# Optimization experiments

Hardware: AMD Instinct MI355X
Metric: run time of the kernel (lower is better)

## Reference

```python
import jax, jax.numpy as jnp
import numpy as np

DIM, INNER, HEADS = 512, 64, 8

def setup_inputs() -> dict:
    key = jax.random.key(0)
    ks = jax.random.split(key, 9)
    s = lambda fan_in: 1.0 / np.sqrt(fan_in)
    x  = jax.random.normal(ks[0], (2, 4096, DIM), dtype=jnp.float32)
    # per-head Q/K/V projection weights (naive per-head linears in the source)
    Wq = jax.random.uniform(ks[1], (HEADS, DIM, INNER), minval=-s(DIM), maxval=s(DIM))
    Wk = jax.random.uniform(ks[2], (HEADS, DIM, INNER), minval=-s(DIM), maxval=s(DIM))
    Wv = jax.random.uniform(ks[3], (HEADS, DIM, INNER), minval=-s(DIM), maxval=s(DIM))
    bq = jax.random.uniform(ks[4], (HEADS, INNER), minval=-s(DIM), maxval=s(DIM))
    bk = jax.random.uniform(ks[5], (HEADS, INNER), minval=-s(DIM), maxval=s(DIM))
    bv = jax.random.uniform(ks[6], (HEADS, INNER), minval=-s(DIM), maxval=s(DIM))
    Wo = jax.random.uniform(ks[7], (HEADS * INNER, DIM), minval=-s(HEADS*INNER), maxval=s(HEADS*INNER))
    bo = jax.random.uniform(ks[8], (DIM,), minval=-s(HEADS*INNER), maxval=s(HEADS*INNER))
    return {"x": x, "Wq": Wq, "bq": bq, "Wk": Wk, "bk": bk, "Wv": Wv, "bv": bv, "Wo": Wo, "bo": bo}

def reference(x, Wq, bq, Wk, bk, Wv, bv, Wo, bo):
    # x: [B,S,D]; per-head projections -> [B,H,S,E]
    q = jnp.einsum('bsd,hde->bhse', x, Wq) + bq[None, :, None, :]
    k = jnp.einsum('bsd,hde->bhse', x, Wk) + bk[None, :, None, :]
    v = jnp.einsum('bsd,hde->bhse', x, Wv) + bv[None, :, None, :]
    scale = 1.0 / jnp.sqrt(jnp.asarray(q.shape[-1], q.dtype))
    scores = jnp.einsum('bhse,bhte->bhst', q, k) * scale  # [B,H,S,S]
    attn = jax.nn.softmax(scores, axis=-1)
    y = jnp.einsum('bhst,bhte->bhse', attn, v)            # [B,H,S,E]
    B, H, S, E = y.shape
    cat = jnp.transpose(y, (0, 2, 1, 3)).reshape(B, S, H * E)
    return cat @ Wo + bo
```

## Files before the change

kernel.cpp:

```cpp
#include <hip/hip_runtime.h>
#include <hip/hip_bf16.h>

typedef __attribute__((ext_vector_type(8))) short bf16x8;
typedef __attribute__((ext_vector_type(4))) float f32x4;
typedef __attribute__((ext_vector_type(16))) float f32x16;
typedef __attribute__((ext_vector_type(4))) unsigned int u32x4;

#define DIM   512
#define INNER 64
#define HEADS 8
#define BATCH 2
#define SEQ   4096
#define MTOT  (BATCH*SEQ)

__device__ __forceinline__ unsigned short f2bf(float f) {
    union { float f; unsigned u; } v; v.f = f;
    unsigned u = v.u;
    unsigned r = (u + 0x7fffu + ((u >> 16) & 1u)) >> 16;
    return (unsigned short)r;
}

__device__ __forceinline__ float bf2f(unsigned short u) {
    union { unsigned u; float f; } v; v.u = ((unsigned)u) << 16;
    return v.f;
}

__device__ __forceinline__ unsigned cvt_pk_bf16(float a, float b) {
    unsigned r;
    asm("v_cvt_pk_bf16_f32 %0, %1, %2" : "=v"(r) : "v"(a), "v"(b));
    return r;
}

#define GLOAD_LDS16(gptr, lptr)                                               \
    __builtin_amdgcn_global_load_lds(                                         \
        (const __attribute__((address_space(1))) unsigned int*)(gptr),        \
        (__attribute__((address_space(3))) unsigned int*)(lptr), 16, 0, 0)

__global__ void convert_kernel(const float* __restrict__ x,
                               const float* __restrict__ Wq,
                               const float* __restrict__ Wk,
                               const float* __restrict__ Wv,
                               const float* __restrict__ Wo,
                               unsigned short* __restrict__ xb,
                               unsigned short* __restrict__ wt,
                               unsigned short* __restrict__ wot) {
    const int total_x = MTOT * DIM / 4;
    const int total_w = 1536 * 512;
    const int total_o = 512 * 512;
    const int total   = total_x + total_w + total_o;
    for (int i = blockIdx.x * blockDim.x + threadIdx.x; i < total;
         i += gridDim.x * blockDim.x) {
        if (i < total_x) {
            float4 v = ((const float4*)x)[i];
            ushort4 o4;
            o4.x = f2bf(v.x); o4.y = f2bf(v.y); o4.z = f2bf(v.z); o4.w = f2bf(v.w);
            ((ushort4*)xb)[i] = o4;
        } else if (i < total_x + total_w) {
            int j = i - total_x;
            int n = j >> 9, d = j & 511;
            int proj = n >> 9, h = (n >> 6) & 7, e = n & 63;
            const float* W = (proj == 0) ? Wq : (proj == 1) ? Wk : Wv;
            wt[j] = f2bf(W[((size_t)h * 512 + d) * 64 + e]);
        } else {
            int j = i - total_x - total_w;
            int n = j >> 9, d = j & 511;
            wot[j] = f2bf(Wo[(size_t)d * 512 + n]);
        }
    }
}

__global__ __launch_bounds__(256) void qkv_gemm(
        const unsigned short* __restrict__ xb,
        const unsigned short* __restrict__ wt,
        const float* __restrict__ bq, const float* __restrict__ bk,
        const float* __restrict__ bv,
        unsigned short* __restrict__ Q, unsigned short* __restrict__ K,
        unsigned short* __restrict__ VT) {
    __shared__ __align__(16) unsigned short As[128][64];
    __shared__ __align__(16) unsigned short Bs[128][64];
    const int m0 = blockIdx.x * 128;
    const int n0 = blockIdx.y * 128;
    const int tid = threadIdx.x;
    const int w = tid >> 6, l = tid & 63;
    const int wm = w >> 1, wn = w & 1;
    const int srow = l >> 3;
    const int cs = (l & 7) ^ srow;
    const unsigned short* aSrc = xb + (size_t)(m0 + w * 32 + srow) * 512 + cs * 8;
    const unsigned short* bSrc = wt + (size_t)(n0 + w * 32 + srow) * 512 + cs * 8;
    f32x4 acc[4][4] = {};

    for (int k0 = 0; k0 < 512; k0 += 64) {
        __syncthreads();
        #pragma unroll
        for (int g = 0; g < 4; ++g) {
            GLOAD_LDS16(aSrc + (size_t)g * 8 * 512 + k0, &As[w * 32 + g * 8][0]);
            GLOAD_LDS16(bSrc + (size_t)g * 8 * 512 + k0, &Bs[w * 32 + g * 8][0]);
        }
        __syncthreads();
        #pragma unroll
        for (int ks = 0; ks < 2; ++ks) {
            const int ccol = (((ks * 4 + (l >> 4)) ^ (l & 7))) * 8;
            bf16x8 a[4], bb[4];
            #pragma unroll
            for (int mb = 0; mb < 4; ++mb)
                a[mb] = *(const bf16x8*)(&As[wm * 64 + mb * 16 + (l & 15)][ccol]);
            #pragma unroll
            for (int nb = 0; nb < 4; ++nb)
                bb[nb] = *(const bf16x8*)(&Bs[wn * 64 + nb * 16 + (l & 15)][ccol]);
            #pragma unroll
            for (int mb = 0; mb < 4; ++mb)
                #pragma unroll
                for (int nb = 0; nb < 4; ++nb)
                    acc[mb][nb] = __builtin_amdgcn_mfma_f32_16x16x32_bf16(
                        a[mb], bb[nb], acc[mb][nb], 0, 0, 0);
        }
    }

    const float QSCALE = 0.125f * 1.4426950408889634f;
    for (int nb = 0; nb < 4; ++nb) {
        int n = n0 + wn * 64 + nb * 16 + (l & 15);
        int proj = n >> 9, h = (n >> 6) & 7, e = n & 63;
        const float* bias = (proj == 0) ? bq : (proj == 1) ? bk : bv;
        float bval = bias[h * 64 + e];
        float scl = (proj == 0) ? QSCALE : 1.0f;
        for (int mb = 0; mb < 4; ++mb) {
            for (int r = 0; r < 4; ++r) {
                int m = m0 + wm * 64 + mb * 16 + (l >> 4) * 4 + r;
                int b = m >> 12, s = m & 4095;
                unsigned short bf = f2bf((acc[mb][nb][r] + bval) * scl);
                if (proj == 0)
                    Q[((size_t)(b * 8 + h) * 4096 + s) * 64 + e] = bf;
                else if (proj == 1)
                    K[((size_t)(b * 8 + h) * 4096 + s) * 64 + e] = bf;
                else
                    VT[((size_t)(b * 8 + h) * 64 + e) * 4096 + s] = bf;
            }
        }
    }
}

template <int NSPLIT>
__global__ __launch_bounds__(256, 4) void flash_attn(
        const unsigned short* __restrict__ Q,
        const unsigned short* __restrict__ K,
        const unsigned short* __restrict__ VT,
        unsigned short* __restrict__ y,
        unsigned short* __restrict__ Opart,
        float* __restrict__ Lpart) {
    __shared__ __align__(16) unsigned short Ks[2][64][64];
    __shared__ __align__(16) unsigned short Vs[2][64][64];

    const int bh = blockIdx.y;
    const int q0 = blockIdx.x * 128;
    const int z = (NSPLIT > 1) ? blockIdx.z : 0;
    const int TPS = 64 / NSPLIT;
    const int t0 = z * TPS;
    const int tid = threadIdx.x;
    const int w = tid >> 6, l = tid & 63;
    const int ql = l & 31, hi = l >> 5;

    const unsigned short* Qp = Q + (size_t)bh * (4096 * 64);
    const unsigned short* Kp = K + (size_t)bh * (4096 * 64);
    const unsigned short* Vp = VT + (size_t)bh * (64 * 4096);

    bf16x8 qf[4];
    const int qrow = q0 + w * 32 + ql;
    #pragma unroll
    for (int i = 0; i < 4; ++i)
        qf[i] = *(const bf16x8*)(Qp + (size_t)qrow * 64 + i * 16 + hi * 8);

    const int srow = l >> 3;
    const int cs = (l & 7) ^ srow;
    const unsigned short* kSrc0 =
        Kp + ((size_t)t0 * 64 + w * 16 + srow) * 64 + cs * 8;
    const unsigned short* kSrc1 = kSrc0 + 8 * 64;
    const unsigned short* vSrc0 =
        Vp + (size_t)(w * 16 + srow) * 4096 + t0 * 64 + cs * 8;
    const unsigned short* vSrc1 = vSrc0 + 8 * 4096;

    f32x16 o[2] = {};
    float ls0 = 0.f, ls1 = 0.f, ls2 = 0.f, ls3 = 0.f;

    GLOAD_LDS16(kSrc0, &Ks[0][w * 16 + 0][0]);
    GLOAD_LDS16(kSrc1, &Ks[0][w * 16 + 8][0]);
    GLOAD_LDS16(vSrc0, &Vs[0][w * 16 + 0][0]);
    GLOAD_LDS16(vSrc1, &Vs[0][w * 16 + 8][0]);
    __syncthreads();

    for (int tt = 0; tt < TPS; ++tt) {
        const int b = tt & 1;
        if (tt < TPS - 1) {
            const size_t ko = (size_t)(tt + 1) * 4096;
            const size_t vo = (size_t)(tt + 1) * 64;
            GLOAD_LDS16(kSrc0 + ko, &Ks[b ^ 1][w * 16 + 0][0]);
            GLOAD_LDS16(kSrc1 + ko, &Ks[b ^ 1][w * 16 + 8][0]);
            GLOAD_LDS16(vSrc0 + vo, &Vs[b ^ 1][w * 16 + 0][0]);
            GLOAD_LDS16(vSrc1 + vo, &Vs[b ^ 1][w * 16 + 8][0]);
        }

        #pragma unroll
        for (int kb = 0; kb < 2; ++kb) {
            f32x16 sA = {};
            __builtin_amdgcn_s_setprio(1);
            #pragma unroll
            for (int i = 0; i < 4; ++i) {
                const int chunk = (2 * i + hi) ^ (l & 7);
                bf16x8 kf = *(const bf16x8*)(&Ks[b][kb * 32 + ql][chunk * 8]);
                sA = __builtin_amdgcn_mfma_f32_32x32x16_bf16(kf, qf[i], sA,
                                                             0, 0, 0);
            }
            __builtin_amdgcn_s_setprio(0);

            #pragma unroll
            for (int r = 0; r < 16; r += 4) {
                float p0 = __builtin_amdgcn_exp2f(sA[r + 0]);
                float p1 = __builtin_amdgcn_exp2f(sA[r + 1]);
                float p2 = __builtin_amdgcn_exp2f(sA[r + 2]);
                float p3 = __builtin_amdgcn_exp2f(sA[r + 3]);
                sA[r + 0] = p0; sA[r + 1] = p1; sA[r + 2] = p2; sA[r + 3] = p3;
                ls0 += p0; ls1 += p1; ls2 += p2; ls3 += p3;
            }

            bf16x8 pf0, pf1;
            {
                unsigned a0 = cvt_pk_bf16(sA[0], sA[1]);
                unsigned a1 = cvt_pk_bf16(sA[2], sA[3]);
                unsigned b0 = cvt_pk_bf16(sA[4], sA[5]);
                unsigned b1 = cvt_pk_bf16(sA[6], sA[7]);
                unsigned c0 = cvt_pk_bf16(sA[8], sA[9]);
                unsigned c1 = cvt_pk_bf16(sA[10], sA[11]);
                unsigned d0 = cvt_pk_bf16(sA[12], sA[13]);
                unsigned d1 = cvt_pk_bf16(sA[14], sA[15]);
#if __has_builtin(__builtin_amdgcn_permlane32_swap)
                auto r0 = __builtin_amdgcn_permlane32_swap(a0, b0, false, false);
                auto r1 = __builtin_amdgcn_permlane32_swap(a1, b1, false, false);
                auto r2 = __builtin_amdgcn_permlane32_swap(c0, d0, false, false);
                auto r3 = __builtin_amdgcn_permlane32_swap(c1, d1, false, false);
                u32x4 w0; w0[0] = r0[0]; w0[1] = r1[0]; w0[2] = r0[1]; w0[3] = r1[1];
                u32x4 w1; w1[0] = r2[0]; w1[1] = r3[0]; w1[2] = r2[1]; w1[3] = r3[1];
#else
                unsigned pa0 = (unsigned)__shfl_xor((int)a0, 32);
                unsigned pb0 = (unsigned)__shfl_xor((int)b0, 32);
                unsigned pa1 = (unsigned)__shfl_xor((int)a1, 32);
                unsigned pb1 = (unsigned)__shfl_xor((int)b1, 32);
                unsigned pc0 = (unsigned)__shfl_xor((int)c0, 32);
                unsigned pd0 = (unsigned)__shfl_xor((int)d0, 32);
                unsigned pc1 = (unsigned)__shfl_xor((int)c1, 32);
                unsigned pd1 = (unsigned)__shfl_xor((int)d1, 32);
                u32x4 w0, w1;
                w0[0] = hi ? pb0 : a0;  w0[1] = hi ? pb1 : a1;
                w0[2] = hi ? b0 : pa0;  w0[3] = hi ? b1 : pa1;
                w1[0] = hi ? pd0 : c0;  w1[1] = hi ? pd1 : c1;
                w1[2] = hi ? d0 : pc0;  w1[3] = hi ? d1 : pc1;
#endif
                pf0 = __builtin_bit_cast(bf16x8, w0);
                pf1 = __builtin_bit_cast(bf16x8, w1);
            }

            __builtin_amdgcn_s_setprio(1);
            #pragma unroll
            for (int eb = 0; eb < 2; ++eb) {
                const int c0i = (2 * (kb * 2 + 0) + hi) ^ (l & 7);
                const int c1i = (2 * (kb * 2 + 1) + hi) ^ (l & 7);
                bf16x8 vf0 = *(const bf16x8*)(&Vs[b][eb * 32 + ql][c0i * 8]);
                o[eb] = __builtin_amdgcn_mfma_f32_32x32x16_bf16(vf0, pf0, o[eb],
                                                                0, 0, 0);
                bf16x8 vf1 = *(const bf16x8*)(&Vs[b][eb * 32 + ql][c1i * 8]);
                o[eb] = __builtin_amdgcn_mfma_f32_32x32x16_bf16(vf1, pf1, o[eb],
                                                                0, 0, 0);
            }
            __builtin_amdgcn_s_setprio(0);
        }

        __syncthreads();
    }

    float lsum = (ls0 + ls1) + (ls2 + ls3);
    lsum += __shfl_xor(lsum, 32);

    if constexpr (NSPLIT == 1) {
        const float inv = 1.0f / lsum;
        const int bb = bh >> 3, h = bh & 7;
        unsigned short* yp = y + ((size_t)(bb * 4096 + qrow)) * 512 + h * 64;
        #pragma unroll
        for (int eb = 0; eb < 2; ++eb) {
            #pragma unroll
            for (int quad = 0; quad < 4; ++quad) {
                ushort4 pk4;
                pk4.x = f2bf(o[eb][quad * 4 + 0] * inv);
                pk4.y = f2bf(o[eb][quad * 4 + 1] * inv);
                pk4.z = f2bf(o[eb][quad * 4 + 2] * inv);
                pk4.w = f2bf(o[eb][quad * 4 + 3] * inv);
                *(ushort4*)(yp + eb * 32 + quad * 8 + hi * 4) = pk4;
            }
        }
    } else {
        const size_t prow = (size_t)z * 65536 + (size_t)bh * 4096 + qrow;
        unsigned short* op = Opart + prow * 64;
        #pragma unroll
        for (int eb = 0; eb < 2; ++eb) {
            #pragma unroll
            for (int quad = 0; quad < 4; ++quad) {
                ushort4 pk4;
                pk4.x = f2bf(o[eb][quad * 4 + 0]);
                pk4.y = f2bf(o[eb][quad * 4 + 1]);
                pk4.z = f2bf(o[eb][quad * 4 + 2]);
                pk4.w = f2bf(o[eb][quad * 4 + 3]);
                *(ushort4*)(op + eb * 32 + quad * 8 + hi * 4) = pk4;
            }
        }
        if (hi == 0) Lpart[prow] = lsum;
    }
}

template <int N>
__global__ __launch_bounds__(256) void merge_kernel(
        const unsigned short* __restrict__ Opart,
        const float* __restrict__ Lpart,
        unsigned short* __restrict__ y) {
    const int gid = blockIdx.x * 256 + threadIdx.x;
    const int row = gid >> 3;
    const int ev = gid & 7;
    float L = 0.f;
    #pragma unroll
    for (int zz = 0; zz < N; ++zz) L += Lpart[(size_t)zz * 65536 + row];
    float acc[8] = {};
    #pragma unroll
    for (int zz = 0; zz < N; ++zz) {
        const ushort4* op =
            (const ushort4*)(Opart + ((size_t)zz * 65536 + row) * 64 + ev * 8);
        ushort4 oa = op[0], ob = op[1];
        acc[0] += bf2f(oa.x); acc[1] += bf2f(oa.y);
        acc[2] += bf2f(oa.z); acc[3] += bf2f(oa.w);
        acc[4] += bf2f(ob.x); acc[5] += bf2f(ob.y);
        acc[6] += bf2f(ob.z); acc[7] += bf2f(ob.w);
    }
    const float inv = 1.0f / L;
    ushort4 ra, rb;
    ra.x = f2bf(acc[0] * inv); ra.y = f2bf(acc[1] * inv);
    ra.z = f2bf(acc[2] * inv); ra.w = f2bf(acc[3] * inv);
    rb.x = f2bf(acc[4] * inv); rb.y = f2bf(acc[5] * inv);
    rb.z = f2bf(acc[6] * inv); rb.w = f2bf(acc[7] * inv);
    const int bh = row >> 12, s = row & 4095;
    const int bb = bh >> 3, h = bh & 7;
    unsigned short* yp =
        y + ((size_t)(bb * 4096 + s)) * 512 + h * 64 + ev * 8;
    ((ushort4*)yp)[0] = ra;
    ((ushort4*)yp)[1] = rb;
}

__global__ __launch_bounds__(256) void out_gemm(
        const unsigned short* __restrict__ yb,
        const unsigned short* __restrict__ wot,
        const float* __restrict__ bo,
        float* __restrict__ out) {
    __shared__ __align__(16) unsigned short As[128][64];
    __shared__ __align__(16) unsigned short Bs[128][64];
    const int m0 = blockIdx.x * 128;
    const int n0 = blockIdx.y * 128;
    const int tid = threadIdx.x;
    const int w = tid >> 6, l = tid & 63;
    const int wm = w >> 1, wn = w & 1;
    const int srow = l >> 3;
    const int cs = (l & 7) ^ srow;
    const unsigned short* aSrc = yb + (size_t)(m0 + w * 32 + srow) * 512 + cs * 8;
    const unsigned short* bSrc = wot + (size_t)(n0 + w * 32 + srow) * 512 + cs * 8;
    f32x4 acc[4][4] = {};

    for (int k0 = 0; k0 < 512; k0 += 64) {
        __syncthreads();
        #pragma unroll
        for (int g = 0; g < 4; ++g) {
            GLOAD_LDS16(aSrc + (size_t)g * 8 * 512 + k0, &As[w * 32 + g * 8][0]);
            GLOAD_LDS16(bSrc + (size_t)g * 8 * 512 + k0, &Bs[w * 32 + g * 8][0]);
        }
        __syncthreads();
        #pragma unroll
        for (int ks = 0; ks < 2; ++ks) {
            const int ccol = (((ks * 4 + (l >> 4)) ^ (l & 7))) * 8;
            bf16x8 a[4], bb[4];
            #pragma unroll
            for (int mb = 0; mb < 4; ++mb)
                a[mb] = *(const bf16x8*)(&As[wm * 64 + mb * 16 + (l & 15)][ccol]);
            #pragma unroll
            for (int nb = 0; nb < 4; ++nb)
                bb[nb] = *(const bf16x8*)(&Bs[wn * 64 + nb * 16 + (l & 15)][ccol]);
            #pragma unroll
            for (int mb = 0; mb < 4; ++mb)
                #pragma unroll
                for (int nb = 0; nb < 4; ++nb)
                    acc[mb][nb] = __builtin_amdgcn_mfma_f32_16x16x32_bf16(
                        a[mb], bb[nb], acc[mb][nb], 0, 0, 0);
        }
    }

    for (int nb = 0; nb < 4; ++nb) {
        int n = n0 + wn * 64 + nb * 16 + (l & 15);
        float bval = bo[n];
        for (int mb = 0; mb < 4; ++mb) {
            for (int r = 0; r < 4; ++r) {
                int m = m0 + wm * 64 + mb * 16 + (l >> 4) * 4 + r;
                out[(size_t)m * 512 + n] = acc[mb][nb][r] + bval;
            }
        }
    }
}

extern "C" void kernel_launch(void* const* d_in, const int* in_sizes, int n_in,
                              void* d_out, int out_size, void* d_ws,
                              size_t ws_size, hipStream_t stream) {
    const float* x  = (const float*)d_in[0];
    const float* Wq = (const float*)d_in[1];
    const float* bq = (const float*)d_in[2];
    const float* Wk = (const float*)d_in[3];
    const float* bk = (const float*)d_in[4];
    const float* Wv = (const float*)d_in[5];
    const float* bv = (const float*)d_in[6];
    const float* Wo = (const float*)d_in[7];
    const float* bo = (const float*)d_in[8];
    float* out = (float*)d_out;

    char* ws = (char*)d_ws;
    unsigned short* xb  = (unsigned short*)(ws);
    unsigned short* wt  = (unsigned short*)(ws + 8388608);
    unsigned short* wot = (unsigned short*)(ws + 9961472);
    unsigned short* Qb  = (unsigned short*)(ws + 10485760);
    unsigned short* Kb  = (unsigned short*)(ws + 18874368);
    unsigned short* VTb = (unsigned short*)(ws + 27262976);
    unsigned short* yb  = (unsigned short*)(ws + 35651584);
    float* Lpart = (float*)(ws + 44040192);
    unsigned short* Opart = (unsigned short*)(ws + 45088768);
    const size_t need4 = 45088768 + 4ull * 8388608;
    const size_t need2 = 45088768 + 2ull * 8388608;

    hipLaunchKernelGGL(convert_kernel, dim3(1024), dim3(256), 0, stream,
                       x, Wq, Wk, Wv, Wo, xb, wt, wot);
    hipLaunchKernelGGL(qkv_gemm, dim3(64, 12), dim3(256), 0, stream,
                       xb, wt, bq, bk, bv, Qb, Kb, VTb);
    if (ws_size >= need4) {
        hipLaunchKernelGGL((flash_attn<4>), dim3(32, 16, 4), dim3(256), 0,
                           stream, Qb, Kb, VTb, yb, Opart, Lpart);
        hipLaunchKernelGGL((merge_kernel<4>), dim3(2048), dim3(256), 0, stream,
                           Opart, Lpart, yb);
    } else if (ws_size >= need2) {
        hipLaunchKernelGGL((flash_attn<2>), dim3(32, 16, 2), dim3(256), 0,
                           stream, Qb, Kb, VTb, yb, Opart, Lpart);
        hipLaunchKernelGGL((merge_kernel<2>), dim3(2048), dim3(256), 0, stream,
                           Opart, Lpart, yb);
    } else {
        hipLaunchKernelGGL((flash_attn<1>), dim3(32, 16, 1), dim3(256), 0,
                           stream, Qb, Kb, VTb, yb, (unsigned short*)nullptr,
                           (float*)nullptr);
    }
    hipLaunchKernelGGL(out_gemm, dim3(64, 4), dim3(256), 0, stream,
                       yb, wot, bo, out);
}
```

Baseline: 144.6 us.

## Process two 32-row query tiles per wave to reuse K/V fragments

Each wave now handles 64 query rows (two 32-row sets) instead of 32, so every K and V fragment loaded from shared memory feeds two MFMA chains. The block's query tile grows from 128 to 256 rows, the grid's x dimension is halved, and launch bounds drop from 4 to 3 waves per EU to leave room for the doubled accumulators and Q fragments. This cuts LDS reads and per-tile global K/V traffic per query, at the cost of higher register pressure, lower occupancy and half as many blocks.

```diff
diff --git a/kernel.cpp b/kernel.cpp
--- a/kernel.cpp
+++ b/kernel.cpp
@@ -140,7 +140,7 @@
 }
 
 template <int NSPLIT>
-__global__ __launch_bounds__(256, 4) void flash_attn(
+__global__ __launch_bounds__(256, 3) void flash_attn(
         const unsigned short* __restrict__ Q,
         const unsigned short* __restrict__ K,
         const unsigned short* __restrict__ VT,
@@ -151,7 +151,7 @@
     __shared__ __align__(16) unsigned short Vs[2][64][64];
 
     const int bh = blockIdx.y;
-    const int q0 = blockIdx.x * 128;
+    const int q0 = blockIdx.x * 256;
     const int z = (NSPLIT > 1) ? blockIdx.z : 0;
     const int TPS = 64 / NSPLIT;
     const int t0 = z * TPS;
@@ -163,11 +163,13 @@
     const unsigned short* Kp = K + (size_t)bh * (4096 * 64);
     const unsigned short* Vp = VT + (size_t)bh * (64 * 4096);
 
-    bf16x8 qf[4];
-    const int qrow = q0 + w * 32 + ql;
+    bf16x8 qf0[4], qf1[4];
+    const int qrow0 = q0 + w * 64 + ql;
     #pragma unroll
-    for (int i = 0; i < 4; ++i)
-        qf[i] = *(const bf16x8*)(Qp + (size_t)qrow * 64 + i * 16 + hi * 8);
+    for (int i = 0; i < 4; ++i) {
+        qf0[i] = *(const bf16x8*)(Qp + (size_t)qrow0 * 64 + i * 16 + hi * 8);
+        qf1[i] = *(const bf16x8*)(Qp + (size_t)(qrow0 + 32) * 64 + i * 16 + hi * 8);
+    }
 
     const int srow = l >> 3;
     const int cs = (l & 7) ^ srow;
@@ -178,8 +180,8 @@
         Vp + (size_t)(w * 16 + srow) * 4096 + t0 * 64 + cs * 8;
     const unsigned short* vSrc1 = vSrc0 + 8 * 4096;
 
-    f32x16 o[2] = {};
-    float ls0 = 0.f, ls1 = 0.f, ls2 = 0.f, ls3 = 0.f;
+    f32x16 o0[2] = {}, o1[2] = {};
+    float lsA = 0.f, lsB = 0.f;
 
     GLOAD_LDS16(kSrc0, &Ks[0][w * 16 + 0][0]);
     GLOAD_LDS16(kSrc1, &Ks[0][w * 16 + 8][0]);
@@ -200,116 +202,144 @@
 
         #pragma unroll
         for (int kb = 0; kb < 2; ++kb) {
-            f32x16 sA = {};
-            __builtin_amdgcn_s_setprio(1);
+            bf16x8 kf[4];
             #pragma unroll
             for (int i = 0; i < 4; ++i) {
                 const int chunk = (2 * i + hi) ^ (l & 7);
-                bf16x8 kf = *(const bf16x8*)(&Ks[b][kb * 32 + ql][chunk * 8]);
-                sA = __builtin_amdgcn_mfma_f32_32x32x16_bf16(kf, qf[i], sA,
-                                                             0, 0, 0);
-            }
+                kf[i] = *(const bf16x8*)(&Ks[b][kb * 32 + ql][chunk * 8]);
+            }
+            f32x16 sA0 = {}, sA1 = {};
+            __builtin_amdgcn_s_setprio(1);
+            #pragma unroll
+            for (int i = 0; i < 4; ++i)
+                sA0 = __builtin_amdgcn_mfma_f32_32x32x16_bf16(kf[i], qf0[i],
+                                                              sA0, 0, 0, 0);
+            #pragma unroll
+            for (int i = 0; i < 4; ++i)
+                sA1 = __builtin_amdgcn_mfma_f32_32x32x16_bf16(kf[i], qf1[i],
+                                                              sA1, 0, 0, 0);
             __builtin_amdgcn_s_setprio(0);
 
-            #pragma unroll
-            for (int r = 0; r < 16; r += 4) {
-                float p0 = __builtin_amdgcn_exp2f(sA[r + 0]);
-                float p1 = __builtin_amdgcn_exp2f(sA[r + 1]);
-                float p2 = __builtin_amdgcn_exp2f(sA[r + 2]);
-                float p3 = __builtin_amdgcn_exp2f(sA[r + 3]);
-                sA[r + 0] = p0; sA[r + 1] = p1; sA[r + 2] = p2; sA[r + 3] = p3;
-                ls0 += p0; ls1 += p1; ls2 += p2; ls3 += p3;
-            }
-
-            bf16x8 pf0, pf1;
-            {
-                unsigned a0 = cvt_pk_bf16(sA[0], sA[1]);
-                unsigned a1 = cvt_pk_bf16(sA[2], sA[3]);
-                unsigned b0 = cvt_pk_bf16(sA[4], sA[5]);
-                unsigned b1 = cvt_pk_bf16(sA[6], sA[7]);
-                unsigned c0 = cvt_pk_bf16(sA[8], sA[9]);
-                unsigned c1 = cvt_pk_bf16(sA[10], sA[11]);
-                unsigned d0 = cvt_pk_bf16(sA[12], sA[13]);
-                unsigned d1 = cvt_pk_bf16(sA[14], sA[15]);
+            bf16x8 vf[4];
+            #pragma unroll
+            for (int eb = 0; eb < 2; ++eb)
+                #pragma unroll
+                for (int j = 0; j < 2; ++j) {
+                    const int chunk = (2 * (kb * 2 + j) + hi) ^ (l & 7);
+                    vf[eb * 2 + j] =
+                        *(const bf16x8*)(&Vs[b][eb * 32 + ql][chunk * 8]);
+                }
+
+            #pragma unroll
+            for (int set = 0; set < 2; ++set) {
+                f32x16& sA = set ? sA1 : sA0;
+                float s0 = 0.f, s1 = 0.f, s2 = 0.f, s3 = 0.f;
+                #pragma unroll
+                for (int r = 0; r < 16; r += 4) {
+                    float p0 = __builtin_amdgcn_exp2f(sA[r + 0]);
+                    float p1 = __builtin_amdgcn_exp2f(sA[r + 1]);
+                    float p2 = __builtin_amdgcn_exp2f(sA[r + 2]);
+                    float p3 = __builtin_amdgcn_exp2f(sA[r + 3]);
+                    sA[r + 0] = p0; sA[r + 1] = p1;
+                    sA[r + 2] = p2; sA[r + 3] = p3;
+                    s0 += p0; s1 += p1; s2 += p2; s3 += p3;
+                }
+                if (set) lsB += (s0 + s1) + (s2 + s3);
+                else     lsA += (s0 + s1) + (s2 + s3);
+
+                bf16x8 pf0, pf1;
+                {
+                    unsigned a0 = cvt_pk_bf16(sA[0], sA[1]);
+                    unsigned a1 = cvt_pk_bf16(sA[2], sA[3]);
+                    unsigned b0 = cvt_pk_bf16(sA[4], sA[5]);
+                    unsigned b1 = cvt_pk_bf16(sA[6], sA[7]);
+                    unsigned c0 = cvt_pk_bf16(sA[8], sA[9]);
+                    unsigned c1 = cvt_pk_bf16(sA[10], sA[11]);
+                    unsigned d0 = cvt_pk_bf16(sA[12], sA[13]);
+                    unsigned d1 = cvt_pk_bf16(sA[14], sA[15]);
 #if __has_builtin(__builtin_amdgcn_permlane32_swap)
-                auto r0 = __builtin_amdgcn_permlane32_swap(a0, b0, false, false);
-                auto r1 = __builtin_amdgcn_permlane32_swap(a1, b1, false, false);
-                auto r2 = __builtin_amdgcn_permlane32_swap(c0, d0, false, false);
-                auto r3 = __builtin_amdgcn_permlane32_swap(c1, d1, false, false);
-                u32x4 w0; w0[0] = r0[0]; w0[1] = r1[0]; w0[2] = r0[1]; w0[3] = r1[1];
-                u32x4 w1; w1[0] = r2[0]; w1[1] = r3[0]; w1[2] = r2[1]; w1[3] = r3[1];
+                    auto r0 = __builtin_amdgcn_permlane32_swap(a0, b0, false, false);
+                    auto r1 = __builtin_amdgcn_permlane32_swap(a1, b1, false, false);
+                    auto r2 = __builtin_amdgcn_permlane32_swap(c0, d0, false, false);
+                    auto r3 = __builtin_amdgcn_permlane32_swap(c1, d1, false, false);
+                    u32x4 w0; w0[0] = r0[0]; w0[1] = r1[0]; w0[2] = r0[1]; w0[3] = r1[1];
+                    u32x4 w1; w1[0] = r2[0]; w1[1] = r3[0]; w1[2] = r2[1]; w1[3] = r3[1];
 #else
-                unsigned pa0 = (unsigned)__shfl_xor((int)a0, 32);
-                unsigned pb0 = (unsigned)__shfl_xor((int)b0, 32);
-                unsigned pa1 = (unsigned)__shfl_xor((int)a1, 32);
-                unsigned pb1 = (unsigned)__shfl_xor((int)b1, 32);
-                unsigned pc0 = (unsigned)__shfl_xor((int)c0, 32);
-                unsigned pd0 = (unsigned)__shfl_xor((int)d0, 32);
-                unsigned pc1 = (unsigned)__shfl_xor((int)c1, 32);
-                unsigned pd1 = (unsigned)__shfl_xor((int)d1, 32);
-                u32x4 w0, w1;
-                w0[0] = hi ? pb0 : a0;  w0[1] = hi ? pb1 : a1;
-                w0[2] = hi ? b0 : pa0;  w0[3] = hi ? b1 : pa1;
-                w1[0] = hi ? pd0 : c0;  w1[1] = hi ? pd1 : c1;
-                w1[2] = hi ? d0 : pc0;  w1[3] = hi ? d1 : pc1;
+                    unsigned pa0 = (unsigned)__shfl_xor((int)a0, 32);
+                    unsigned pb0 = (unsigned)__shfl_xor((int)b0, 32);
+                    unsigned pa1 = (unsigned)__shfl_xor((int)a1, 32);
+                    unsigned pb1 = (unsigned)__shfl_xor((int)b1, 32);
+                    unsigned pc0 = (unsigned)__shfl_xor((int)c0, 32);
+                    unsigned pd0 = (unsigned)__shfl_xor((int)d0, 32);
+                    unsigned pc1 = (unsigned)__shfl_xor((int)c1, 32);
+                    unsigned pd1 = (unsigned)__shfl_xor((int)d1, 32);
+                    u32x4 w0, w1;
+                    w0[0] = hi ? pb0 : a0;  w0[1] = hi ? pb1 : a1;
+                    w0[2] = hi ? b0 : pa0;  w0[3] = hi ? b1 : pa1;
+                    w1[0] = hi ? pd0 : c0;  w1[1] = hi ? pd1 : c1;
+                    w1[2] = hi ? d0 : pc0;  w1[3] = hi ? d1 : pc1;
 #endif
-                pf0 = __builtin_bit_cast(bf16x8, w0);
-                pf1 = __builtin_bit_cast(bf16x8, w1);
-            }
-
-            __builtin_amdgcn_s_setprio(1);
+                    pf0 = __builtin_bit_cast(bf16x8, w0);
+                    pf1 = __builtin_bit_cast(bf16x8, w1);
+                }
+
+                __builtin_amdgcn_s_setprio(1);
+                #pragma unroll
+                for (int eb = 0; eb < 2; ++eb) {
+                    f32x16& oacc = set ? o1[eb] : o0[eb];
+                    oacc = __builtin_amdgcn_mfma_f32_32x32x16_bf16(
+                        vf[eb * 2 + 0], pf0, oacc, 0, 0, 0);
+                    oacc = __builtin_amdgcn_mfma_f32_32x32x16_bf16(
+                        vf[eb * 2 + 1], pf1, oacc, 0, 0, 0);
+                }
+                __builtin_amdgcn_s_setprio(0);
+            }
+        }
+
+        __syncthreads();
+    }
+
+    #pragma unroll
+    for (int set = 0; set < 2; ++set) {
+        float lsum = set ? lsB : lsA;
+        lsum += __shfl_xor(lsum, 32);
+        const int qrow = qrow0 + set * 32;
+        if constexpr (NSPLIT == 1) {
+            const float inv = 1.0f / lsum;
+            const int bb = bh >> 3, h = bh & 7;
+            unsigned short* yp =
+                y + ((size_t)(bb * 4096 + qrow)) * 512 + h * 64;
             #pragma unroll
             for (int eb = 0; eb < 2; ++eb) {
-                const int c0i = (2 * (kb * 2 + 0) + hi) ^ (l & 7);
-                const int c1i = (2 * (kb * 2 + 1) + hi) ^ (l & 7);
-                bf16x8 vf0 = *(const bf16x8*)(&Vs[b][eb * 32 + ql][c0i * 8]);
-                o[eb] = __builtin_amdgcn_mfma_f32_32x32x16_bf16(vf0, pf0, o[eb],
-                                                                0, 0, 0);
-                bf16x8 vf1 = *(const bf16x8*)(&Vs[b][eb * 32 + ql][c1i * 8]);
-                o[eb] = __builtin_amdgcn_mfma_f32_32x32x16_bf16(vf1, pf1, o[eb],
-                                                                0, 0, 0);
-            }
-            __builtin_amdgcn_s_setprio(0);
-        }
-
-        __syncthreads();
-    }
-
-    float lsum = (ls0 + ls1) + (ls2 + ls3);
-    lsum += __shfl_xor(lsum, 32);
-
-    if constexpr (NSPLIT == 1) {
-        const float inv = 1.0f / lsum;
-        const int bb = bh >> 3, h = bh & 7;
-        unsigned short* yp = y + ((size_t)(bb * 4096 + qrow)) * 512 + h * 64;
-        #pragma unroll
-        for (int eb = 0; eb < 2; ++eb) {
-            #pragma unroll
-            for (int quad = 0; quad < 4; ++quad) {
-                ushort4 pk4;
-                pk4.x = f2bf(o[eb][quad * 4 + 0] * inv);
-                pk4.y = f2bf(o[eb][quad * 4 + 1] * inv);
-                pk4.z = f2bf(o[eb][quad * 4 + 2] * inv);
-                pk4.w = f2bf(o[eb][quad * 4 + 3] * inv);
-                *(ushort4*)(yp + eb * 32 + quad * 8 + hi * 4) = pk4;
-            }
-        }
-    } else {
-        const size_t prow = (size_t)z * 65536 + (size_t)bh * 4096 + qrow;
-        unsigned short* op = Opart + prow * 64;
-        #pragma unroll
-        for (int eb = 0; eb < 2; ++eb) {
-            #pragma unroll
-            for (int quad = 0; quad < 4; ++quad) {
-                ushort4 pk4;
-                pk4.x = f2bf(o[eb][quad * 4 + 0]);
-                pk4.y = f2bf(o[eb][quad * 4 + 1]);
-                pk4.z = f2bf(o[eb][quad * 4 + 2]);
-                pk4.w = f2bf(o[eb][quad * 4 + 3]);
-                *(ushort4*)(op + eb * 32 + quad * 8 + hi * 4) = pk4;
-            }
-        }
-        if (hi == 0) Lpart[prow] = lsum;
+                const f32x16& oacc = set ? o1[eb] : o0[eb];
+                #pragma unroll
+                for (int quad = 0; quad < 4; ++quad) {
+                    ushort4 pk4;
+                    pk4.x = f2bf(oacc[quad * 4 + 0] * inv);
+                    pk4.y = f2bf(oacc[quad * 4 + 1] * inv);
+                    pk4.z = f2bf(oacc[quad * 4 + 2] * inv);
+                    pk4.w = f2bf(oacc[quad * 4 + 3] * inv);
+                    *(ushort4*)(yp + eb * 32 + quad * 8 + hi * 4) = pk4;
+                }
+            }
+        } else {
+            const size_t prow = (size_t)z * 65536 + (size_t)bh * 4096 + qrow;
+            unsigned short* op = Opart + prow * 64;
+            #pragma unroll
+            for (int eb = 0; eb < 2; ++eb) {
+                const f32x16& oacc = set ? o1[eb] : o0[eb];
+                #pragma unroll
+                for (int quad = 0; quad < 4; ++quad) {
+                    ushort4 pk4;
+                    pk4.x = f2bf(oacc[quad * 4 + 0]);
+                    pk4.y = f2bf(oacc[quad * 4 + 1]);
+                    pk4.z = f2bf(oacc[quad * 4 + 2]);
+                    pk4.w = f2bf(oacc[quad * 4 + 3]);
+                    *(ushort4*)(op + eb * 32 + quad * 8 + hi * 4) = pk4;
+                }
+            }
+            if (hi == 0) Lpart[prow] = lsum;
+        }
     }
 }
 
@@ -438,17 +468,17 @@
     hipLaunchKernelGGL(qkv_gemm, dim3(64, 12), dim3(256), 0, stream,
                        xb, wt, bq, bk, bv, Qb, Kb, VTb);
     if (ws_size >= need4) {
-        hipLaunchKernelGGL((flash_attn<4>), dim3(32, 16, 4), dim3(256), 0,
+        hipLaunchKernelGGL((flash_attn<4>), dim3(16, 16, 4), dim3(256), 0,
                            stream, Qb, Kb, VTb, yb, Opart, Lpart);
         hipLaunchKernelGGL((merge_kernel<4>), dim3(2048), dim3(256), 0, stream,
                            Opart, Lpart, yb);
     } else if (ws_size >= need2) {
-        hipLaunchKernelGGL((flash_attn<2>), dim3(32, 16, 2), dim3(256), 0,
+        hipLaunchKernelGGL((flash_attn<2>), dim3(16, 16, 2), dim3(256), 0,
                            stream, Qb, Kb, VTb, yb, Opart, Lpart);
         hipLaunchKernelGGL((merge_kernel<2>), dim3(2048), dim3(256), 0, stream,
                            Opart, Lpart, yb);
     } else {
-        hipLaunchKernelGGL((flash_attn<1>), dim3(32, 16, 1), dim3(256), 0,
+        hipLaunchKernelGGL((flash_attn<1>), dim3(16, 16, 1), dim3(256), 0,
                            stream, Qb, Kb, VTb, yb, (unsigned short*)nullptr,
                            (float*)nullptr);
     }
```

Result: slower. 209.3 us (+44.8%).

## Process two 32-row query tiles per wave to reuse K/V fragments

Applied to the files above, without the earlier changes.

Each wave now handles 64 query rows (two 32-row MFMA tiles) instead of 32, so every K and V fragment read from LDS feeds two sets of MFMAs. The query block per workgroup doubles to 256 rows and the grid halves. The softmax/PV step moves into a helper, and launch bounds drop to 2 waves-per-EU to make room for the extra accumulators. This cuts LDS traffic per FLOP and the number of K/V tile loads, at the cost of more registers, lower occupancy and fewer blocks (512 at the default split).

```diff
diff --git a/kernel.cpp b/kernel.cpp
--- a/kernel.cpp
+++ b/kernel.cpp
@@ -139,8 +139,91 @@
     }
 }
 
+__device__ __forceinline__ void sm_pv(f32x16& sA, float& ls,
+                                      const bf16x8& vf00, const bf16x8& vf01,
+                                      const bf16x8& vf10, const bf16x8& vf11,
+                                      f32x16& oA, f32x16& oB, const int hi) {
+    float s0 = 0.f, s1 = 0.f, s2 = 0.f, s3 = 0.f;
+    #pragma unroll
+    for (int r = 0; r < 16; r += 4) {
+        float p0 = __builtin_amdgcn_exp2f(sA[r + 0]);
+        float p1 = __builtin_amdgcn_exp2f(sA[r + 1]);
+        float p2 = __builtin_amdgcn_exp2f(sA[r + 2]);
+        float p3 = __builtin_amdgcn_exp2f(sA[r + 3]);
+        sA[r + 0] = p0; sA[r + 1] = p1; sA[r + 2] = p2; sA[r + 3] = p3;
+        s0 += p0; s1 += p1; s2 += p2; s3 += p3;
+    }
+    ls += (s0 + s1) + (s2 + s3);
+
+    bf16x8 pf0, pf1;
+    {
+        unsigned a0 = cvt_pk_bf16(sA[0], sA[1]);
+        unsigned a1 = cvt_pk_bf16(sA[2], sA[3]);
+        unsigned b0 = cvt_pk_bf16(sA[4], sA[5]);
+        unsigned b1 = cvt_pk_bf16(sA[6], sA[7]);
+        unsigned c0 = cvt_pk_bf16(sA[8], sA[9]);
+        unsigned c1 = cvt_pk_bf16(sA[10], sA[11]);
+        unsigned d0 = cvt_pk_bf16(sA[12], sA[13]);
+        unsigned d1 = cvt_pk_bf16(sA[14], sA[15]);
+#if __has_builtin(__builtin_amdgcn_permlane32_swap)
+        auto r0 = __builtin_amdgcn_permlane32_swap(a0, b0, false, false);
+        auto r1 = __builtin_amdgcn_permlane32_swap(a1, b1, false, false);
+        auto r2 = __builtin_amdgcn_permlane32_swap(c0, d0, false, false);
+        auto r3 = __builtin_amdgcn_permlane32_swap(c1, d1, false, false);
+        u32x4 w0; w0[0] = r0[0]; w0[1] = r1[0]; w0[2] = r0[1]; w0[3] = r1[1];
+        u32x4 w1; w1[0] = r2[0]; w1[1] = r3[0]; w1[2] = r2[1]; w1[3] = r3[1];
+#else
+        unsigned pa0 = (unsigned)__shfl_xor((int)a0, 32);
+        unsigned pb0 = (unsigned)__shfl_xor((int)b0, 32);
+        unsigned pa1 = (unsigned)__shfl_xor((int)a1, 32);
+        unsigned pb1 = (unsigned)__shfl_xor((int)b1, 32);
+        unsigned pc0 = (unsigned)__shfl_xor((int)c0, 32);
+        unsigned pd0 = (unsigned)__shfl_xor((int)d0, 32);
+        unsigned pc1 = (unsigned)__shfl_xor((int)c1, 32);
+        unsigned pd1 = (unsigned)__shfl_xor((int)d1, 32);
+        u32x4 w0, w1;
+        w0[0] = hi ? pb0 : a0;  w0[1] = hi ? pb1 : a1;
+        w0[2] = hi ? b0 : pa0;  w0[3] = hi ? b1 : pa1;
+        w1[0] = hi ? pd0 : c0;  w1[1] = hi ? pd1 : c1;
+        w1[2] = hi ? d0 : pc0;  w1[3] = hi ? d1 : pc1;
+#endif
+        pf0 = __builtin_bit_cast(bf16x8, w0);
+        pf1 = __builtin_bit_cast(bf16x8, w1);
+    }
+
+    __builtin_amdgcn_s_setprio(1);
+    oA = __builtin_amdgcn_mfma_f32_32x32x16_bf16(vf00, pf0, oA, 0, 0, 0);
+    oA = __builtin_amdgcn_mfma_f32_32x32x16_bf16(vf01, pf1, oA, 0, 0, 0);
+    oB = __builtin_amdgcn_mfma_f32_32x32x16_bf16(vf10, pf0, oB, 0, 0, 0);
+    oB = __builtin_amdgcn_mfma_f32_32x32x16_bf16(vf11, pf1, oB, 0, 0, 0);
+    __builtin_amdgcn_s_setprio(0);
+}
+
+__device__ __forceinline__ void store_o(const f32x16& oA, const f32x16& oB,
+                                        unsigned short* p, float scale,
+                                        int hi) {
+    #pragma unroll
+    for (int quad = 0; quad < 4; ++quad) {
+        ushort4 pk4;
+        pk4.x = f2bf(oA[quad * 4 + 0] * scale);
+        pk4.y = f2bf(oA[quad * 4 + 1] * scale);
+        pk4.z = f2bf(oA[quad * 4 + 2] * scale);
+        pk4.w = f2bf(oA[quad * 4 + 3] * scale);
+        *(ushort4*)(p + quad * 8 + hi * 4) = pk4;
+    }
+    #pragma unroll
+    for (int quad = 0; quad < 4; ++quad) {
+        ushort4 pk4;
+        pk4.x = f2bf(oB[quad * 4 + 0] * scale);
+        pk4.y = f2bf(oB[quad * 4 + 1] * scale);
+        pk4.z = f2bf(oB[quad * 4 + 2] * scale);
+        pk4.w = f2bf(oB[quad * 4 + 3] * scale);
+        *(ushort4*)(p + 32 + quad * 8 + hi * 4) = pk4;
+    }
+}
+
 template <int NSPLIT>
-__global__ __launch_bounds__(256, 4) void flash_attn(
+__global__ __launch_bounds__(256, 2) void flash_attn(
         const unsigned short* __restrict__ Q,
         const unsigned short* __restrict__ K,
         const unsigned short* __restrict__ VT,
@@ -151,7 +234,7 @@
     __shared__ __align__(16) unsigned short Vs[2][64][64];
 
     const int bh = blockIdx.y;
-    const int q0 = blockIdx.x * 128;
+    const int q0 = blockIdx.x * 256;
     const int z = (NSPLIT > 1) ? blockIdx.z : 0;
     const int TPS = 64 / NSPLIT;
     const int t0 = z * TPS;
@@ -163,11 +246,13 @@
     const unsigned short* Kp = K + (size_t)bh * (4096 * 64);
     const unsigned short* Vp = VT + (size_t)bh * (64 * 4096);
 
-    bf16x8 qf[4];
-    const int qrow = q0 + w * 32 + ql;
-    #pragma unroll
-    for (int i = 0; i < 4; ++i)
-        qf[i] = *(const bf16x8*)(Qp + (size_t)qrow * 64 + i * 16 + hi * 8);
+    bf16x8 qf0[4], qf1[4];
+    const int qrow0 = q0 + w * 64 + ql;
+    #pragma unroll
+    for (int i = 0; i < 4; ++i) {
+        qf0[i] = *(const bf16x8*)(Qp + (size_t)qrow0 * 64 + i * 16 + hi * 8);
+        qf1[i] = *(const bf16x8*)(Qp + (size_t)(qrow0 + 32) * 64 + i * 16 + hi * 8);
+    }
 
     const int srow = l >> 3;
     const int cs = (l & 7) ^ srow;
@@ -178,8 +263,8 @@
         Vp + (size_t)(w * 16 + srow) * 4096 + t0 * 64 + cs * 8;
     const unsigned short* vSrc1 = vSrc0 + 8 * 4096;
 
-    f32x16 o[2] = {};
-    float ls0 = 0.f, ls1 = 0.f, ls2 = 0.f, ls3 = 0.f;
+    f32x16 o00 = {}, o01 = {}, o10 = {}, o11 = {};
+    float lsA = 0.f, lsB = 0.f;
 
     GLOAD_LDS16(kSrc0, &Ks[0][w * 16 + 0][0]);
     GLOAD_LDS16(kSrc1, &Ks[0][w * 16 + 8][0]);
@@ -200,116 +285,66 @@
 
         #pragma unroll
         for (int kb = 0; kb < 2; ++kb) {
-            f32x16 sA = {};
+            bf16x8 kf0, kf1, kf2, kf3;
+            {
+                const int c0 = (0 + hi) ^ (l & 7);
+                const int c1 = (2 + hi) ^ (l & 7);
+                const int c2 = (4 + hi) ^ (l & 7);
+                const int c3 = (6 + hi) ^ (l & 7);
+                kf0 = *(const bf16x8*)(&Ks[b][kb * 32 + ql][c0 * 8]);
+                kf1 = *(const bf16x8*)(&Ks[b][kb * 32 + ql][c1 * 8]);
+                kf2 = *(const bf16x8*)(&Ks[b][kb * 32 + ql][c2 * 8]);
+                kf3 = *(const bf16x8*)(&Ks[b][kb * 32 + ql][c3 * 8]);
+            }
+            f32x16 sA0 = {}, sA1 = {};
             __builtin_amdgcn_s_setprio(1);
-            #pragma unroll
-            for (int i = 0; i < 4; ++i) {
-                const int chunk = (2 * i + hi) ^ (l & 7);
-                bf16x8 kf = *(const bf16x8*)(&Ks[b][kb * 32 + ql][chunk * 8]);
-                sA = __builtin_amdgcn_mfma_f32_32x32x16_bf16(kf, qf[i], sA,
-                                                             0, 0, 0);
+            sA0 = __builtin_amdgcn_mfma_f32_32x32x16_bf16(kf0, qf0[0], sA0, 0, 0, 0);
+            sA0 = __builtin_amdgcn_mfma_f32_32x32x16_bf16(kf1, qf0[1], sA0, 0, 0, 0);
+            sA0 = __builtin_amdgcn_mfma_f32_32x32x16_bf16(kf2, qf0[2], sA0, 0, 0, 0);
+            sA0 = __builtin_amdgcn_mfma_f32_32x32x16_bf16(kf3, qf0[3], sA0, 0, 0, 0);
+            sA1 = __builtin_amdgcn_mfma_f32_32x32x16_bf16(kf0, qf1[0], sA1, 0, 0, 0);
+            sA1 = __builtin_amdgcn_mfma_f32_32x32x16_bf16(kf1, qf1[1], sA1, 0, 0, 0);
+            sA1 = __builtin_amdgcn_mfma_f32_32x32x16_bf16(kf2, qf1[2], sA1, 0, 0, 0);
+            sA1 = __builtin_amdgcn_mfma_f32_32x32x16_bf16(kf3, qf1[3], sA1, 0, 0, 0);
+            __builtin_amdgcn_s_setprio(0);
+
+            bf16x8 vf00, vf01, vf10, vf11;
+            {
+                const int c0 = (2 * (kb * 2 + 0) + hi) ^ (l & 7);
+                const int c1 = (2 * (kb * 2 + 1) + hi) ^ (l & 7);
+                vf00 = *(const bf16x8*)(&Vs[b][0 * 32 + ql][c0 * 8]);
+                vf01 = *(const bf16x8*)(&Vs[b][0 * 32 + ql][c1 * 8]);
+                vf10 = *(const bf16x8*)(&Vs[b][1 * 32 + ql][c0 * 8]);
+                vf11 = *(const bf16x8*)(&Vs[b][1 * 32 + ql][c1 * 8]);
             }
-            __builtin_amdgcn_s_setprio(0);
-
-            #pragma unroll
-            for (int r = 0; r < 16; r += 4) {
-                float p0 = __builtin_amdgcn_exp2f(sA[r + 0]);
-                float p1 = __builtin_amdgcn_exp2f(sA[r + 1]);
-                float p2 = __builtin_amdgcn_exp2f(sA[r + 2]);
-                float p3 = __builtin_amdgcn_exp2f(sA[r + 3]);
-                sA[r + 0] = p0; sA[r + 1] = p1; sA[r + 2] = p2; sA[r + 3] = p3;
-                ls0 += p0; ls1 += p1; ls2 += p2; ls3 += p3;
-            }
-
-            bf16x8 pf0, pf1;
-            {
-                unsigned a0 = cvt_pk_bf16(sA[0], sA[1]);
-                unsigned a1 = cvt_pk_bf16(sA[2], sA[3]);
-                unsigned b0 = cvt_pk_bf16(sA[4], sA[5]);
-                unsigned b1 = cvt_pk_bf16(sA[6], sA[7]);
-                unsigned c0 = cvt_pk_bf16(sA[8], sA[9]);
-                unsigned c1 = cvt_pk_bf16(sA[10], sA[11]);
-                unsigned d0 = cvt_pk_bf16(sA[12], sA[13]);
-                unsigned d1 = cvt_pk_bf16(sA[14], sA[15]);
-#if __has_builtin(__builtin_amdgcn_permlane32_swap)
-                auto r0 = __builtin_amdgcn_permlane32_swap(a0, b0, false, false);
-                auto r1 = __builtin_amdgcn_permlane32_swap(a1, b1, false, false);
-                auto r2 = __builtin_amdgcn_permlane32_swap(c0, d0, false, false);
-                auto r3 = __builtin_amdgcn_permlane32_swap(c1, d1, false, false);
-                u32x4 w0; w0[0] = r0[0]; w0[1] = r1[0]; w0[2] = r0[1]; w0[3] = r1[1];
-                u32x4 w1; w1[0] = r2[0]; w1[1] = r3[0]; w1[2] = r2[1]; w1[3] = r3[1];
-#else
-                unsigned pa0 = (unsigned)__shfl_xor((int)a0, 32);
-                unsigned pb0 = (unsigned)__shfl_xor((int)b0, 32);
-                unsigned pa1 = (unsigned)__shfl_xor((int)a1, 32);
-                unsigned pb1 = (unsigned)__shfl_xor((int)b1, 32);
-                unsigned pc0 = (unsigned)__shfl_xor((int)c0, 32);
-                unsigned pd0 = (unsigned)__shfl_xor((int)d0, 32);
-                unsigned pc1 = (unsigned)__shfl_xor((int)c1, 32);
-                unsigned pd1 = (unsigned)__shfl_xor((int)d1, 32);
-                u32x4 w0, w1;
-                w0[0] = hi ? pb0 : a0;  w0[1] = hi ? pb1 : a1;
-                w0[2] = hi ? b0 : pa0;  w0[3] = hi ? b1 : pa1;
-                w1[0] = hi ? pd0 : c0;  w1[1] = hi ? pd1 : c1;
-                w1[2] = hi ? d0 : pc0;  w1[3] = hi ? d1 : pc1;
-#endif
-                pf0 = __builtin_bit_cast(bf16x8, w0);
-                pf1 = __builtin_bit_cast(bf16x8, w1);
-            }
-
-            __builtin_amdgcn_s_setprio(1);
-            #pragma unroll
-            for (int eb = 0; eb < 2; ++eb) {
-                const int c0i = (2 * (kb * 2 + 0) + hi) ^ (l & 7);
-                const int c1i = (2 * (kb * 2 + 1) + hi) ^ (l & 7);
-                bf16x8 vf0 = *(const bf16x8*)(&Vs[b][eb * 32 + ql][c0i * 8]);
-                o[eb] = __builtin_amdgcn_mfma_f32_32x32x16_bf16(vf0, pf0, o[eb],
-                                                                0, 0, 0);
-                bf16x8 vf1 = *(const bf16x8*)(&Vs[b][eb * 32 + ql][c1i * 8]);
-                o[eb] = __builtin_amdgcn_mfma_f32_32x32x16_bf16(vf1, pf1, o[eb],
-                                                                0, 0, 0);
-            }
-            __builtin_amdgcn_s_setprio(0);
+
+            sm_pv(sA0, lsA, vf00, vf01, vf10, vf11, o00, o01, hi);
+            sm_pv(sA1, lsB, vf00, vf01, vf10, vf11, o10, o11, hi);
         }
 
         __syncthreads();
     }
 
-    float lsum = (ls0 + ls1) + (ls2 + ls3);
-    lsum += __shfl_xor(lsum, 32);
+    float lsum0 = lsA + __shfl_xor(lsA, 32);
+    float lsum1 = lsB + __shfl_xor(lsB, 32);
 
     if constexpr (NSPLIT == 1) {
-        const float inv = 1.0f / lsum;
         const int bb = bh >> 3, h = bh & 7;
-        unsigned short* yp = y + ((size_t)(bb * 4096 + qrow)) * 512 + h * 64;
-        #pragma unroll
-        for (int eb = 0; eb < 2; ++eb) {
-            #pragma unroll
-            for (int quad = 0; quad < 4; ++quad) {
-                ushort4 pk4;
-                pk4.x = f2bf(o[eb][quad * 4 + 0] * inv);
-                pk4.y = f2bf(o[eb][quad * 4 + 1] * inv);
-                pk4.z = f2bf(o[eb][quad * 4 + 2] * inv);
-                pk4.w = f2bf(o[eb][quad * 4 + 3] * inv);
-                *(ushort4*)(yp + eb * 32 + quad * 8 + hi * 4) = pk4;
-            }
-        }
+        unsigned short* yp0 =
+            y + ((size_t)(bb * 4096 + qrow0)) * 512 + h * 64;
+        unsigned short* yp1 =
+            y + ((size_t)(bb * 4096 + qrow0 + 32)) * 512 + h * 64;
+        store_o(o00, o01, yp0, 1.0f / lsum0, hi);
+        store_o(o10, o11, yp1, 1.0f / lsum1, hi);
     } else {
-        const size_t prow = (size_t)z * 65536 + (size_t)bh * 4096 + qrow;
-        unsigned short* op = Opart + prow * 64;
-        #pragma unroll
-        for (int eb = 0; eb < 2; ++eb) {
-            #pragma unroll
-            for (int quad = 0; quad < 4; ++quad) {
-                ushort4 pk4;
-                pk4.x = f2bf(o[eb][quad * 4 + 0]);
-                pk4.y = f2bf(o[eb][quad * 4 + 1]);
-                pk4.z = f2bf(o[eb][quad * 4 + 2]);
-                pk4.w = f2bf(o[eb][quad * 4 + 3]);
-                *(ushort4*)(op + eb * 32 + quad * 8 + hi * 4) = pk4;
-            }
-        }
-        if (hi == 0) Lpart[prow] = lsum;
+        const size_t prow0 = (size_t)z * 65536 + (size_t)bh * 4096 + qrow0;
+        const size_t prow1 = prow0 + 32;
+        store_o(o00, o01, Opart + prow0 * 64, 1.0f, hi);
+        store_o(o10, o11, Opart + prow1 * 64, 1.0f, hi);
+        if (hi == 0) {
+            Lpart[prow0] = lsum0;
+            Lpart[prow1] = lsum1;
+        }
     }
 }
 
@@ -438,17 +473,17 @@
     hipLaunchKernelGGL(qkv_gemm, dim3(64, 12), dim3(256), 0, stream,
                        xb, wt, bq, bk, bv, Qb, Kb, VTb);
     if (ws_size >= need4) {
-        hipLaunchKernelGGL((flash_attn<4>), dim3(32, 16, 4), dim3(256), 0,
+        hipLaunchKernelGGL((flash_attn<4>), dim3(16, 16, 4), dim3(256), 0,
                            stream, Qb, Kb, VTb, yb, Opart, Lpart);
         hipLaunchKernelGGL((merge_kernel<4>), dim3(2048), dim3(256), 0, stream,
                            Opart, Lpart, yb);
     } else if (ws_size >= need2) {
-        hipLaunchKernelGGL((flash_attn<2>), dim3(32, 16, 2), dim3(256), 0,
+        hipLaunchKernelGGL((flash_attn<2>), dim3(16, 16, 2), dim3(256), 0,
                            stream, Qb, Kb, VTb, yb, Opart, Lpart);
         hipLaunchKernelGGL((merge_kernel<2>), dim3(2048), dim3(256), 0, stream,
                            Opart, Lpart, yb);
     } else {
-        hipLaunchKernelGGL((flash_attn<1>), dim3(32, 16, 1), dim3(256), 0,
+        hipLaunchKernelGGL((flash_attn<1>), dim3(16, 16, 1), dim3(256), 0,
                            stream, Qb, Kb, VTb, yb, (unsigned short*)nullptr,
                            (float*)nullptr);
     }
```

New measurement: 142.8 us. Within noise of the previous version (-1.3%).
